# Optimization experiments

Hardware: AMD Instinct MI355X
Metric: run time of the kernel (lower is better)

Reference implementation:

```python
import jax, jax.numpy as jnp
import numpy as np
from jax import lax

ROUNDS = 64
HIDDEN = 256
BATCH = 16384


def setup_inputs() -> dict:
    key = jax.random.key(0)
    k1, k2, k3 = jax.random.split(key, 3)
    # state: (B, 256) bits in {0,1} as float32 (output of bytes_to_bits)
    state = jax.random.bernoulli(k1, 0.5, (BATCH, HIDDEN)).astype(jnp.float32)
    # matrices: (64, 256, 256) ternary values in {-1,0,1} (byte % 3 - 1)
    matrices = jax.random.randint(k2, (ROUNDS, HIDDEN, HIDDEN), -1, 2).astype(jnp.float32)
    # noise: (B, 64, 256) bits in {0,1} derived from sha256 of the nonce
    noise = jax.random.bernoulli(k3, 0.5, (BATCH, ROUNDS, HIDDEN)).astype(jnp.float32)
    return {"state": state, "matrices": matrices, "noise": noise}


def reference(state, matrices, noise):
    # 64-round recurrence: s <- (floor(s @ M_r^T + n_r)) mod 2
    noise_r = jnp.transpose(noise, (1, 0, 2))  # (R, B, H)

    def step(s, xs):
        M, n = xs  # M: (H,H), n: (B,H)
        s = jnp.remainder(jnp.floor(s @ M.T + n), 2.0)
        return s, None

    final, _ = lax.scan(step, state, (matrices, noise_r))
    return final  # (B, 256) bits as float32
```

## Files before the change

kernel.cpp:

```cpp
#include <hip/hip_runtime.h>

typedef unsigned int u32;
typedef unsigned long long u64;

#define R_ROUNDS 64
#define HID 256
#define BATCH 16384
#define RPW 4


__global__ __launch_bounds__(256) void pack_matrices_kernel(
        const float* __restrict__ M, u32* __restrict__ P) {
    const int lane = threadIdx.x & 63;
    const int row  = (int)((blockIdx.x * blockDim.x + threadIdx.x) >> 6);
    const float4 v = *(const float4*)(M + (size_t)row * HID + 4 * lane);
    const u64 b0 = __ballot(v.x != 0.0f);
    const u64 b1 = __ballot(v.y != 0.0f);
    const u64 b2 = __ballot(v.z != 0.0f);
    const u64 b3 = __ballot(v.w != 0.0f);
    if (lane < 8) {
        const int i = lane >> 1;
        u64 bb = b0;
        if (i == 1) bb = b1;
        if (i == 2) bb = b2;
        if (i == 3) bb = b3;
        P[row * 8 + lane] = (lane & 1) ? (u32)(bb >> 32) : (u32)bb;
    }
}

__global__ __launch_bounds__(256, 4) void tenshash_kernel(
        const float* __restrict__ state,
        const u32*  __restrict__ pA,
        const float* __restrict__ noise,
        float* __restrict__ out) {
    const int lane = threadIdx.x & 63;
    const int warp = threadIdx.x >> 6;
    const int wave = (int)(blockIdx.x * 4 + warp);
    const int row0 = wave * RPW;

    __shared__ u32 smem[2][2048];

    u64 S0[RPW], S1[RPW], S2[RPW], S3[RPW];
#pragma unroll
    for (int rw = 0; rw < RPW; ++rw) {
        const float4 v = *(const float4*)(state + (size_t)(row0 + rw) * HID + 4 * lane);
        S0[rw] = __ballot(v.x != 0.0f);
        S1[rw] = __ballot(v.y != 0.0f);
        S2[rw] = __ballot(v.z != 0.0f);
        S3[rw] = __ballot(v.w != 0.0f);
    }

    const float* no_l = noise + (size_t)row0 * (R_ROUNDS * HID) + 4 * lane;

    const int sa = lane >> 3, sb = lane & 7;
    const int src_chunk_lo = (sa << 3) + (sb ^ sa);
    auto STAGE = [&](int r, int b) {
        if (warp == 0) {
            const char* g = (const char*)(pA + (size_t)r * 2048);
#pragma unroll
            for (int t = 0; t < 8; ++t) {
                __builtin_amdgcn_global_load_lds(
                    (const __attribute__((address_space(1))) void*)
                        (g + t * 1024 + src_chunk_lo * 16),
                    (__attribute__((address_space(3))) void*)&smem[b][t * 256],
                    16, 0, 0);
            }
        }
    };
    auto LOADN = [&](float4* n, int r) {
#pragma unroll
        for (int rw = 0; rw < RPW; ++rw)
            n[rw] = *(const float4*)(no_l + (size_t)rw * (R_ROUNDS * HID) + r * HID);
    };
    auto RUN = [&](int b, const float4* n) {
        const uint4* p = (const uint4*)&smem[b][0];
        uint4 a[8];
#pragma unroll
        for (int t = 0; t < 8; ++t)
            a[t] = p[(lane << 3) + (t ^ (lane & 7))];
#pragma unroll
        for (int rw = 0; rw < RPW; ++rw) {
            u64 ns0, ns1, ns2, ns3;
#pragma unroll
            for (int i = 0; i < 4; ++i) {
                const u64 W0 = (u64)a[2 * i].x     | ((u64)a[2 * i].y     << 32);
                const u64 W1 = (u64)a[2 * i].z     | ((u64)a[2 * i].w     << 32);
                const u64 W2 = (u64)a[2 * i + 1].x | ((u64)a[2 * i + 1].y << 32);
                const u64 W3 = (u64)a[2 * i + 1].z | ((u64)a[2 * i + 1].w << 32);
                const float nfv = (i == 0) ? n[rw].x : (i == 1) ? n[rw].y
                                : (i == 2) ? n[rw].z : n[rw].w;
                const u32 c = (u32)__popcll(W0 & S0[rw]) + (u32)__popcll(W1 & S1[rw])
                            + (u32)__popcll(W2 & S2[rw]) + (u32)__popcll(W3 & S3[rw])
                            + (u32)nfv;
                const u64 nb = __ballot((c & 1u) != 0);
                if (i == 0) ns0 = nb; else if (i == 1) ns1 = nb;
                else if (i == 2) ns2 = nb; else ns3 = nb;
            }
            S0[rw] = ns0; S1[rw] = ns1; S2[rw] = ns2; S3[rw] = ns3;
        }
    };

    float4 nA[RPW], nB[RPW];
    STAGE(0, 0);
    LOADN(nA, 0);
    __syncthreads();
#pragma unroll 1
    for (int r = 0; r < R_ROUNDS; r += 2) {
        STAGE(r + 1, 1);
        LOADN(nB, r + 1);
        RUN(0, nA);
        __syncthreads();
        if (r + 2 < R_ROUNDS) {
            STAGE(r + 2, 0);
            LOADN(nA, r + 2);
        }
        RUN(1, nB);
        __syncthreads();
    }

#pragma unroll
    for (int rw = 0; rw < RPW; ++rw) {
        float4 o;
        o.x = (float)((u32)(S0[rw] >> lane) & 1u);
        o.y = (float)((u32)(S1[rw] >> lane) & 1u);
        o.z = (float)((u32)(S2[rw] >> lane) & 1u);
        o.w = (float)((u32)(S3[rw] >> lane) & 1u);
        *(float4*)(out + (size_t)(row0 + rw) * HID + 4 * lane) = o;
    }
}

extern "C" void kernel_launch(void* const* d_in, const int* in_sizes, int n_in,
                              void* d_out, int out_size, void* d_ws, size_t ws_size,
                              hipStream_t stream) {
    const float* state = (const float*)d_in[0];
    const float* mats  = (const float*)d_in[1];
    const float* noise = (const float*)d_in[2];
    float* out         = (float*)d_out;
    u32* pA            = (u32*)d_ws;

    pack_matrices_kernel<<<(R_ROUNDS * HID) / 4, 256, 0, stream>>>(mats, pA);

    const int blocks = (BATCH / RPW) / 4;
    tenshash_kernel<<<blocks, 256, 0, stream>>>(state, pA, noise, out);
}
```

Measured before the change: 230.6 us.

## Deepen matrix staging to a 4-buffer ring and spread DMA across all warps

The shared-memory matrix buffer grows from double to quadruple buffering, so each round's packed matrix is prefetched two rounds ahead. The global-to-LDS copy work is split across all four warps instead of only warp 0. Full __syncthreads are replaced by a raw s_barrier plus a hand-placed vmcnt wait and scheduling barriers, aiming to cut per-round synchronisation stalls and load latency. This doubles LDS use per block, which may reduce occupancy. It also depends on the manual wait counts being correct for the asynchronous LDS loads.

```diff
diff --git a/kernel.cpp b/kernel.cpp
--- a/kernel.cpp
+++ b/kernel.cpp
@@ -38,7 +38,7 @@
     const int wave = (int)(blockIdx.x * 4 + warp);
     const int row0 = wave * RPW;
 
-    __shared__ u32 smem[2][2048];
+    __shared__ u32 smem[4][2048];
 
     u64 S0[RPW], S1[RPW], S2[RPW], S3[RPW];
 #pragma unroll
@@ -55,16 +55,14 @@
     const int sa = lane >> 3, sb = lane & 7;
     const int src_chunk_lo = (sa << 3) + (sb ^ sa);
     auto STAGE = [&](int r, int b) {
-        if (warp == 0) {
-            const char* g = (const char*)(pA + (size_t)r * 2048);
+        const char* g = (const char*)(pA + (size_t)r * 2048);
 #pragma unroll
-            for (int t = 0; t < 8; ++t) {
-                __builtin_amdgcn_global_load_lds(
-                    (const __attribute__((address_space(1))) void*)
-                        (g + t * 1024 + src_chunk_lo * 16),
-                    (__attribute__((address_space(3))) void*)&smem[b][t * 256],
-                    16, 0, 0);
-            }
+        for (int t = 2 * warp; t < 2 * warp + 2; ++t) {
+            __builtin_amdgcn_global_load_lds(
+                (const __attribute__((address_space(1))) void*)
+                    (g + t * 1024 + src_chunk_lo * 16),
+                (__attribute__((address_space(3))) void*)&smem[b][t * 256],
+                16, 0, 0);
         }
     };
     auto LOADN = [&](float4* n, int r) {
@@ -72,8 +70,8 @@
         for (int rw = 0; rw < RPW; ++rw)
             n[rw] = *(const float4*)(no_l + (size_t)rw * (R_ROUNDS * HID) + r * HID);
     };
-    auto RUN = [&](int b, const float4* n) {
-        const uint4* p = (const uint4*)&smem[b][0];
+    auto RUN = [&](const u32* sb_, const float4* n) {
+        const uint4* p = (const uint4*)sb_;
         uint4 a[8];
 #pragma unroll
         for (int t = 0; t < 8; ++t)
@@ -101,22 +99,34 @@
     };
 
     float4 nA[RPW], nB[RPW];
+
     STAGE(0, 0);
+    STAGE(1, 1);
+    __builtin_amdgcn_sched_barrier(0);
+    asm volatile("" ::: "memory");
     LOADN(nA, 0);
-    __syncthreads();
+    asm volatile("s_waitcnt vmcnt(4)" ::: "memory");
+    __builtin_amdgcn_sched_barrier(0);
+
+#define SUBROUND(k, BUFS, NUSE, NLOAD)                                   \
+    asm volatile("" ::: "memory");                                       \
+    __builtin_amdgcn_s_barrier();                                        \
+    asm volatile("" ::: "memory");                                       \
+    if (r + k + 2 < R_ROUNDS) STAGE(r + k + 2, BUFS);                    \
+    __builtin_amdgcn_sched_barrier(0);                                   \
+    asm volatile("" ::: "memory");                                       \
+    { int rn = r + k + 1; if (rn > R_ROUNDS - 1) rn = R_ROUNDS - 1;      \
+      LOADN(NLOAD, rn); }                                                \
+    RUN(&smem[k][0], NUSE);
+
 #pragma unroll 1
-    for (int r = 0; r < R_ROUNDS; r += 2) {
-        STAGE(r + 1, 1);
-        LOADN(nB, r + 1);
-        RUN(0, nA);
-        __syncthreads();
-        if (r + 2 < R_ROUNDS) {
-            STAGE(r + 2, 0);
-            LOADN(nA, r + 2);
-        }
-        RUN(1, nB);
-        __syncthreads();
+    for (int r = 0; r < R_ROUNDS; r += 4) {
+        SUBROUND(0, 2, nA, nB)
+        SUBROUND(1, 3, nB, nA)
+        SUBROUND(2, 0, nA, nB)
+        SUBROUND(3, 1, nB, nA)
     }
+#undef SUBROUND
 
 #pragma unroll
     for (int rw = 0; rw < RPW; ++rw) {
```

Result: slower. 458.6 us (+98.9%).

## Stage two rounds of packed matrices per barrier and split staging across warps

Applied to the files above, without the earlier changes.

The pipeline now stages two consecutive rounds' packed matrices (16 KB) into each LDS buffer, with all four waves issuing the global-to-LDS copies instead of only wave 0. Two rounds are run between barriers, which halves the number of __syncthreads calls. Noise prefetch now runs two rounds ahead. This doubles LDS use to 32 KB per block, which may cut occupancy, and holds more noise registers. Loads past the last round are clamped to valid indices and simply reload data that is never used.

```diff
diff --git a/kernel.cpp b/kernel.cpp
--- a/kernel.cpp
+++ b/kernel.cpp
@@ -38,7 +38,7 @@
     const int wave = (int)(blockIdx.x * 4 + warp);
     const int row0 = wave * RPW;
 
-    __shared__ u32 smem[2][2048];
+    __shared__ u32 smem[2][4096];
 
     u64 S0[RPW], S1[RPW], S2[RPW], S3[RPW];
 #pragma unroll
@@ -54,17 +54,16 @@
 
     const int sa = lane >> 3, sb = lane & 7;
     const int src_chunk_lo = (sa << 3) + (sb ^ sa);
-    auto STAGE = [&](int r, int b) {
-        if (warp == 0) {
-            const char* g = (const char*)(pA + (size_t)r * 2048);
+
+    auto STAGE = [&](int q, int b) {
+        const char* g = (const char*)(pA + (size_t)q * 2048);
 #pragma unroll
-            for (int t = 0; t < 8; ++t) {
-                __builtin_amdgcn_global_load_lds(
-                    (const __attribute__((address_space(1))) void*)
-                        (g + t * 1024 + src_chunk_lo * 16),
-                    (__attribute__((address_space(3))) void*)&smem[b][t * 256],
-                    16, 0, 0);
-            }
+        for (int t = 4 * warp; t < 4 * warp + 4; ++t) {
+            __builtin_amdgcn_global_load_lds(
+                (const __attribute__((address_space(1))) void*)
+                    (g + t * 1024 + src_chunk_lo * 16),
+                (__attribute__((address_space(3))) void*)&smem[b][t * 256],
+                16, 0, 0);
         }
     };
     auto LOADN = [&](float4* n, int r) {
@@ -72,8 +71,8 @@
         for (int rw = 0; rw < RPW; ++rw)
             n[rw] = *(const float4*)(no_l + (size_t)rw * (R_ROUNDS * HID) + r * HID);
     };
-    auto RUN = [&](int b, const float4* n) {
-        const uint4* p = (const uint4*)&smem[b][0];
+    auto RUN = [&](const u32* base, const float4* n) {
+        const uint4* p = (const uint4*)base;
         uint4 a[8];
 #pragma unroll
         for (int t = 0; t < 8; ++t)
@@ -100,21 +99,34 @@
         }
     };
 
-    float4 nA[RPW], nB[RPW];
+    float4 n0[RPW], n1[RPW], n2[RPW], n3[RPW];
+
+    LOADN(n0, 0);
+    LOADN(n1, 1);
     STAGE(0, 0);
-    LOADN(nA, 0);
     __syncthreads();
+
 #pragma unroll 1
-    for (int r = 0; r < R_ROUNDS; r += 2) {
-        STAGE(r + 1, 1);
-        LOADN(nB, r + 1);
-        RUN(0, nA);
+    for (int r = 0; r < R_ROUNDS; r += 4) {
+        LOADN(n2, r + 2);
+        LOADN(n3, r + 3);
+        STAGE(r + 2, 1);
+        RUN(&smem[0][0],    n0);
+        RUN(&smem[0][2048], n1);
         __syncthreads();
-        if (r + 2 < R_ROUNDS) {
-            STAGE(r + 2, 0);
-            LOADN(nA, r + 2);
+
+        {
+            const int ra = (r + 4 > 63) ? 63 : r + 4;
+            const int rb = (r + 5 > 63) ? 63 : r + 5;
+            LOADN(n0, ra);
+            LOADN(n1, rb);
         }
-        RUN(1, nB);
+        {
+            const int q = (r + 4 > 62) ? 62 : r + 4;
+            STAGE(q, 0);
+        }
+        RUN(&smem[1][0],    n2);
+        RUN(&smem[1][2048], n3);
         __syncthreads();
     }
 
```

Result: slower. 248.7 us (+7.9%).

## Halve rows per wave, raise occupancy, and split matrix staging across warps

Applied to the files above, without the earlier changes.

Rows per wave drop from 4 to 2, which doubles the block count, and the launch bound asks for 8 blocks per SM instead of 4. The inner loop is reordered so each pair of matrix chunks is read from LDS and used for all rows before the next pair is loaded, which lowers register pressure. Loading each round's matrix into LDS is now shared by all four warps instead of only warp 0. The kernel is mostly bound by streaming the noise tensor, so the goal is better latency hiding. The cost is twice as much matrix traffic from L2, since each matrix is now reused by half as many rows.

```diff
diff --git a/kernel.cpp b/kernel.cpp
--- a/kernel.cpp
+++ b/kernel.cpp
@@ -6,7 +6,7 @@
 #define R_ROUNDS 64
 #define HID 256
 #define BATCH 16384
-#define RPW 4
+#define RPW 2
 
 
 __global__ __launch_bounds__(256) void pack_matrices_kernel(
@@ -28,7 +28,7 @@
     }
 }
 
-__global__ __launch_bounds__(256, 4) void tenshash_kernel(
+__global__ __launch_bounds__(256, 8) void tenshash_kernel(
         const float* __restrict__ state,
         const u32*  __restrict__ pA,
         const float* __restrict__ noise,
@@ -40,31 +40,30 @@
 
     __shared__ u32 smem[2][2048];
 
-    u64 S0[RPW], S1[RPW], S2[RPW], S3[RPW];
+    u64 S[RPW][4];
 #pragma unroll
     for (int rw = 0; rw < RPW; ++rw) {
         const float4 v = *(const float4*)(state + (size_t)(row0 + rw) * HID + 4 * lane);
-        S0[rw] = __ballot(v.x != 0.0f);
-        S1[rw] = __ballot(v.y != 0.0f);
-        S2[rw] = __ballot(v.z != 0.0f);
-        S3[rw] = __ballot(v.w != 0.0f);
+        S[rw][0] = __ballot(v.x != 0.0f);
+        S[rw][1] = __ballot(v.y != 0.0f);
+        S[rw][2] = __ballot(v.z != 0.0f);
+        S[rw][3] = __ballot(v.w != 0.0f);
     }
 
     const float* no_l = noise + (size_t)row0 * (R_ROUNDS * HID) + 4 * lane;
 
     const int sa = lane >> 3, sb = lane & 7;
     const int src_chunk_lo = (sa << 3) + (sb ^ sa);
+
     auto STAGE = [&](int r, int b) {
-        if (warp == 0) {
-            const char* g = (const char*)(pA + (size_t)r * 2048);
+        const char* g = (const char*)(pA + (size_t)r * 2048);
 #pragma unroll
-            for (int t = 0; t < 8; ++t) {
-                __builtin_amdgcn_global_load_lds(
-                    (const __attribute__((address_space(1))) void*)
-                        (g + t * 1024 + src_chunk_lo * 16),
-                    (__attribute__((address_space(3))) void*)&smem[b][t * 256],
-                    16, 0, 0);
-            }
+        for (int t = 2 * warp; t < 2 * warp + 2; ++t) {
+            __builtin_amdgcn_global_load_lds(
+                (const __attribute__((address_space(1))) void*)
+                    (g + t * 1024 + src_chunk_lo * 16),
+                (__attribute__((address_space(3))) void*)&smem[b][t * 256],
+                16, 0, 0);
         }
     };
     auto LOADN = [&](float4* n, int r) {
@@ -72,35 +71,35 @@
         for (int rw = 0; rw < RPW; ++rw)
             n[rw] = *(const float4*)(no_l + (size_t)rw * (R_ROUNDS * HID) + r * HID);
     };
-    auto RUN = [&](int b, const float4* n) {
-        const uint4* p = (const uint4*)&smem[b][0];
-        uint4 a[8];
+    auto RUN = [&](const u32* base, const float4* n) {
+        const uint4* p = (const uint4*)base;
+        u64 ns[RPW][4];
 #pragma unroll
-        for (int t = 0; t < 8; ++t)
-            a[t] = p[(lane << 3) + (t ^ (lane & 7))];
+        for (int i = 0; i < 4; ++i) {
+            const uint4 a0 = p[(lane << 3) + ((2 * i)     ^ (lane & 7))];
+            const uint4 a1 = p[(lane << 3) + ((2 * i + 1) ^ (lane & 7))];
+            const u64 W0 = (u64)a0.x | ((u64)a0.y << 32);
+            const u64 W1 = (u64)a0.z | ((u64)a0.w << 32);
+            const u64 W2 = (u64)a1.x | ((u64)a1.y << 32);
+            const u64 W3 = (u64)a1.z | ((u64)a1.w << 32);
 #pragma unroll
-        for (int rw = 0; rw < RPW; ++rw) {
-            u64 ns0, ns1, ns2, ns3;
-#pragma unroll
-            for (int i = 0; i < 4; ++i) {
-                const u64 W0 = (u64)a[2 * i].x     | ((u64)a[2 * i].y     << 32);
-                const u64 W1 = (u64)a[2 * i].z     | ((u64)a[2 * i].w     << 32);
-                const u64 W2 = (u64)a[2 * i + 1].x | ((u64)a[2 * i + 1].y << 32);
-                const u64 W3 = (u64)a[2 * i + 1].z | ((u64)a[2 * i + 1].w << 32);
+            for (int rw = 0; rw < RPW; ++rw) {
                 const float nfv = (i == 0) ? n[rw].x : (i == 1) ? n[rw].y
                                 : (i == 2) ? n[rw].z : n[rw].w;
-                const u32 c = (u32)__popcll(W0 & S0[rw]) + (u32)__popcll(W1 & S1[rw])
-                            + (u32)__popcll(W2 & S2[rw]) + (u32)__popcll(W3 & S3[rw])
+                const u32 c = (u32)__popcll(W0 & S[rw][0]) + (u32)__popcll(W1 & S[rw][1])
+                            + (u32)__popcll(W2 & S[rw][2]) + (u32)__popcll(W3 & S[rw][3])
                             + (u32)nfv;
-                const u64 nb = __ballot((c & 1u) != 0);
-                if (i == 0) ns0 = nb; else if (i == 1) ns1 = nb;
-                else if (i == 2) ns2 = nb; else ns3 = nb;
+                ns[rw][i] = __ballot((c & 1u) != 0);
             }
-            S0[rw] = ns0; S1[rw] = ns1; S2[rw] = ns2; S3[rw] = ns3;
         }
+#pragma unroll
+        for (int rw = 0; rw < RPW; ++rw)
+#pragma unroll
+            for (int k = 0; k < 4; ++k) S[rw][k] = ns[rw][k];
     };
 
     float4 nA[RPW], nB[RPW];
+
     STAGE(0, 0);
     LOADN(nA, 0);
     __syncthreads();
@@ -108,23 +107,23 @@
     for (int r = 0; r < R_ROUNDS; r += 2) {
         STAGE(r + 1, 1);
         LOADN(nB, r + 1);
-        RUN(0, nA);
+        RUN(&smem[0][0], nA);
         __syncthreads();
         if (r + 2 < R_ROUNDS) {
             STAGE(r + 2, 0);
             LOADN(nA, r + 2);
         }
-        RUN(1, nB);
+        RUN(&smem[1][0], nB);
         __syncthreads();
     }
 
 #pragma unroll
     for (int rw = 0; rw < RPW; ++rw) {
         float4 o;
-        o.x = (float)((u32)(S0[rw] >> lane) & 1u);
-        o.y = (float)((u32)(S1[rw] >> lane) & 1u);
-        o.z = (float)((u32)(S2[rw] >> lane) & 1u);
-        o.w = (float)((u32)(S3[rw] >> lane) & 1u);
+        o.x = (float)((u32)(S[rw][0] >> lane) & 1u);
+        o.y = (float)((u32)(S[rw][1] >> lane) & 1u);
+        o.z = (float)((u32)(S[rw][2] >> lane) & 1u);
+        o.w = (float)((u32)(S[rw][3] >> lane) & 1u);
         *(float4*)(out + (size_t)(row0 + rw) * HID + 4 * lane) = o;
     }
 }
```

Measured after the change: 865.8 us. 276% more time.
